# Kernel tuning notes

Hardware: AMD Instinct MI355X
Metric: run time of the kernel (lower is better)

Reference implementation:

```python
import jax, jax.numpy as jnp
import numpy as np

N, D, K = 32768, 256, 2048
BETA = 0.25  # init arg beta, in [0,1) branch of the loss


def setup_inputs() -> dict:
    key = jax.random.key(0)
    k1, k2 = jax.random.split(key)
    x = jax.random.normal(k1, (N, D), dtype=jnp.float32)
    # mimics nn.Embedding init: uniform(-1/K, 1/K) then mean-centered
    cb = jax.random.uniform(k2, (K, D), dtype=jnp.float32, minval=-1.0 / K, maxval=1.0 / K)
    codebook = cb - cb.mean(axis=0)
    return {"x": x, "codebook": codebook}


def reference(x, codebook):
    # pairwise squared L2 distances: [N, K]
    dist = (
        jnp.sum(x * x, axis=1, keepdims=True)
        + jnp.sum(codebook * codebook, axis=1)
        - 2.0 * jnp.matmul(x, codebook.T)
    )
    encoding_inds = jnp.argmin(dist, axis=1)  # [N]
    # one-hot @ codebook == gather of nearest code vectors
    x_codebook = jnp.take(codebook, encoding_inds, axis=0)  # [N, D]
    # straight-through quantization
    x_quantized = x + jax.lax.stop_gradient(x_codebook - x)
    # VQ loss, beta in [0, 1) branch
    commit = jnp.mean((x - jax.lax.stop_gradient(x_codebook)) ** 2)
    embed = jnp.mean((x_codebook - jax.lax.stop_gradient(x)) ** 2)
    loss = BETA * commit + embed
    return x_quantized, loss
```

## Files before the change

### kernel.cpp

```cpp
#include <hip/hip_runtime.h>

#define N_ROWS 32768
#define DIM    256
#define KCODES 2048
#define CSCALE 4096.0f

typedef __attribute__((ext_vector_type(16))) float f32x16;
typedef __attribute__((ext_vector_type(4)))  unsigned int u32x4;

union frag16 { u32x4 v; long l[2]; };

__device__ __forceinline__ void gl16(const void* g, void* l) {
    __builtin_amdgcn_global_load_lds(
        (const __attribute__((address_space(1))) unsigned int*)g,
        (__attribute__((address_space(3))) unsigned int*)l, 16, 0, 0);
}

__device__ __forceinline__ uint4 pack16(const float* s) {
    int a = __builtin_amdgcn_cvt_pk_fp8_f32(s[0],  s[1],  0, false);
    a     = __builtin_amdgcn_cvt_pk_fp8_f32(s[2],  s[3],  a, true);
    int b = __builtin_amdgcn_cvt_pk_fp8_f32(s[4],  s[5],  0, false);
    b     = __builtin_amdgcn_cvt_pk_fp8_f32(s[6],  s[7],  b, true);
    int c = __builtin_amdgcn_cvt_pk_fp8_f32(s[8],  s[9],  0, false);
    c     = __builtin_amdgcn_cvt_pk_fp8_f32(s[10], s[11], c, true);
    int d = __builtin_amdgcn_cvt_pk_fp8_f32(s[12], s[13], 0, false);
    d     = __builtin_amdgcn_cvt_pk_fp8_f32(s[14], s[15], d, true);
    uint4 o; o.x = a; o.y = b; o.z = c; o.w = d;
    return o;
}


__global__ void prep_cb(const float* __restrict__ cb, unsigned int* __restrict__ cbf8,
                        float* __restrict__ halfcn, float* __restrict__ loss) {
    const int t    = threadIdx.x;
    const int code = blockIdx.x * 4 + (t >> 6);
    const int s    = t & 63;
    if (blockIdx.x == 0 && t == 0) *loss = 0.0f;
    const int kc = s >> 4, d = (s >> 2) & 3, b4 = (s & 3) * 4;
    const int h = d >> 1, q = d & 1;
    const int k0 = kc * 64 + q * 32 + (b4 >> 3) * 16 + h * 8 + (b4 & 7);
    float4 v = *(const float4*)&cb[(size_t)code * DIM + k0];
    int pk = __builtin_amdgcn_cvt_pk_fp8_f32(v.x * CSCALE, v.y * CSCALE, 0, false);
    pk     = __builtin_amdgcn_cvt_pk_fp8_f32(v.z * CSCALE, v.w * CSCALE, pk, true);
    cbf8[(size_t)code * 64 + s] = (unsigned int)pk;
    float ssum = v.x * v.x + v.y * v.y + v.z * v.z + v.w * v.w;
    #pragma unroll
    for (int o = 32; o > 0; o >>= 1) ssum += __shfl_down(ssum, o, 64);
    if (s == 0) halfcn[code] = 0.5f * CSCALE * ssum;
}

__global__ __launch_bounds__(256, 3) void vq_fused(
        const float* __restrict__ x, const float* __restrict__ cb,
        const char* __restrict__ cbf8, const float* __restrict__ halfcn,
        float* __restrict__ out, float* __restrict__ loss) {
    __shared__ char As[4][4096];
    __shared__ char Bs[2][16384];
    __shared__ float red[64][4];
    __shared__ int  idxs[64];
    __shared__ float lred[4];

    const int t    = threadIdx.x;
    const int lane = t & 63;
    const int w    = t >> 6;
    const int l32  = lane & 31;
    const int h    = lane >> 5;
    const int row0 = blockIdx.x * 64;

    {
        const int r   = t >> 2;
        const int kc  = t & 3;
        const int key = (r >> 1) & 3;
        const float* src = x + (size_t)(row0 + r) * DIM + kc * 64;
        float buf[16];
        #pragma unroll
        for (int p = 0; p < 4; p++) {
            const int d = p ^ key, hh = d >> 1, qq = d & 1;
            #pragma unroll
            for (int j = 0; j < 4; j++) *(float4*)(buf + j * 4) =
                *(const float4*)(src + qq * 32 + (j >> 1) * 16 + hh * 8 + (j & 1) * 4);
            *(uint4*)(As[kc] + r * 64 + p * 16) = pack16(buf);
        }
    }

    auto stageB = [&](int pass, int kc, char* buf) {
        #pragma unroll
        for (int r_ = 0; r_ < 4; r_++) {
            const int lc = r_ * 64 + w * 16 + (lane >> 2);
            const int g  = (lane & 3) ^ ((lc >> 1) & 3);
            const char* src = cbf8 + (size_t)(pass * 256 + lc) * 256 + kc * 64 + g * 16;
            gl16(src, buf + (r_ * 64 + w * 16) * 64);
        }
    };

    float mp[2][16];
    #pragma unroll
    for (int rt = 0; rt < 2; rt++)
        #pragma unroll
        for (int r = 0; r < 16; r++) mp[rt][r] = -3.0e38f;

    const int key = (l32 >> 1) & 3;
    const int p0  = (h * 2 + 0) ^ key;
    const int p1  = (h * 2 + 1) ^ key;

    stageB(0, 0, Bs[0]);
    int cur = 0;
    for (int pass = 0; pass < 8; ++pass) {
        const float hc0 = halfcn[pass * 256 + w * 64 + l32];
        const float hc1 = halfcn[pass * 256 + w * 64 + 32 + l32];
        f32x16 acc[2][2];
        #pragma unroll
        for (int rt = 0; rt < 2; rt++)
            #pragma unroll
            for (int r = 0; r < 16; r++) { acc[rt][0][r] = -hc0; acc[rt][1][r] = -hc1; }

        #pragma unroll
        for (int kc = 0; kc < 4; ++kc) {
            __syncthreads();
            const int i = pass * 4 + kc;
            if (i < 31) stageB((i + 1) >> 2, (i + 1) & 3, Bs[cur ^ 1]);

            const char* ab = As[kc];
            const char* bb = Bs[cur];
            frag16 af[2][2], bf[2][2];
            #pragma unroll
            for (int rt = 0; rt < 2; rt++) {
                const int rbase = (rt * 32 + l32) * 64;
                af[rt][0].v = *(const u32x4*)(ab + rbase + p0 * 16);
                af[rt][1].v = *(const u32x4*)(ab + rbase + p1 * 16);
            }
            #pragma unroll
            for (int ct = 0; ct < 2; ct++) {
                const int cbase = (w * 64 + ct * 32 + l32) * 64;
                bf[ct][0].v = *(const u32x4*)(bb + cbase + p0 * 16);
                bf[ct][1].v = *(const u32x4*)(bb + cbase + p1 * 16);
            }
            #pragma unroll
            for (int q = 0; q < 2; q++)
                #pragma unroll
                for (int hf = 0; hf < 2; hf++)
                    #pragma unroll
                    for (int rt = 0; rt < 2; rt++)
                        #pragma unroll
                        for (int ct = 0; ct < 2; ct++)
                            acc[rt][ct] = __builtin_amdgcn_mfma_f32_32x32x16_fp8_fp8(
                                af[rt][q].l[hf], bf[ct][q].l[hf], acc[rt][ct], 0, 0, 0);
            cur ^= 1;
        }

        #pragma unroll
        for (int ct = 0; ct < 2; ct++) {
            const unsigned code = (unsigned)(pass * 256 + w * 64 + ct * 32 + l32);
            #pragma unroll
            for (int rt = 0; rt < 2; rt++)
                #pragma unroll
                for (int r = 0; r < 16; r++) {
                    unsigned u = (__float_as_uint(acc[rt][ct][r]) & 0xFFFFF800u) | code;
                    mp[rt][r] = fmaxf(mp[rt][r], __uint_as_float(u));
                }
        }
    }

    #pragma unroll
    for (int m = 1; m <= 16; m <<= 1)
        #pragma unroll
        for (int rt = 0; rt < 2; rt++)
            #pragma unroll
            for (int r = 0; r < 16; r++)
                mp[rt][r] = fmaxf(mp[rt][r], __shfl_xor(mp[rt][r], m, 64));

    if (l32 == 0) {
        #pragma unroll
        for (int rt = 0; rt < 2; rt++)
            #pragma unroll
            for (int r = 0; r < 16; r++) {
                const int row = rt * 32 + (r & 3) + 8 * (r >> 2) + 4 * h;
                red[row][w] = mp[rt][r];
            }
    }
    __syncthreads();
    if (t < 64) {
        float b0 = fmaxf(fmaxf(red[t][0], red[t][1]), fmaxf(red[t][2], red[t][3]));
        idxs[t] = (int)(__float_as_uint(b0) & 2047u);
    }
    __syncthreads();

    float lsum = 0.0f;
    #pragma unroll 4
    for (int r = 0; r < 64; r++) {
        const int code = idxs[r];
        const float c  = cb[(size_t)code * DIM + t];
        const float xv = x[(size_t)(row0 + r) * DIM + t];
        out[(size_t)(row0 + r) * DIM + t] = c;
        const float d = xv - c;
        lsum += d * d;
    }
    #pragma unroll
    for (int o = 32; o > 0; o >>= 1) lsum += __shfl_down(lsum, o, 64);
    if (lane == 0) lred[w] = lsum;
    __syncthreads();
    if (t == 0) {
        const float scale = 1.25f / (float)((size_t)N_ROWS * DIM);
        atomicAdd(loss, (lred[0] + lred[1] + lred[2] + lred[3]) * scale);
    }
}

extern "C" void kernel_launch(void* const* d_in, const int* in_sizes, int n_in,
                              void* d_out, int out_size, void* d_ws, size_t ws_size,
                              hipStream_t stream) {
    const float* x  = (const float*)d_in[0];
    const float* cb = (const float*)d_in[1];
    float* out  = (float*)d_out;
    float* loss = out + (size_t)N_ROWS * DIM;

    char* ws = (char*)d_ws;
    unsigned int* cbf8 = (unsigned int*)ws;
    float* halfcn = (float*)(ws + (size_t)KCODES * 256);

    prep_cb<<<KCODES / 4, 256, 0, stream>>>(cb, cbf8, halfcn, loss);
    vq_fused<<<N_ROWS / 64, 256, 0, stream>>>(x, cb, (const char*)cbf8, halfcn, out, loss);
}
```

Baseline: 126.0 us.

## Give each wave a private codebook slice and replace barriers with waitcnts

Each wave now stages only the 64 codebook rows it consumes into its own LDS region, so the per-k-chunk __syncthreads can be replaced by explicit s_waitcnt on vmcnt/lgkmcnt. The halfcn values for all passes are preloaded into registers up front, and launch bounds drop from 3 to 2 waves per SIMD to make room for the extra registers. The aim is to remove block-wide barrier stalls from the main MFMA loop. In exchange it lowers possible occupancy and depends on hand-encoded waitcnt constants being correct for the double buffer, with no barrier protecting against overwriting a buffer before the LDS reads are done.

```diff
diff --git a/kernel.cpp b/kernel.cpp
--- a/kernel.cpp
+++ b/kernel.cpp
@@ -9,6 +9,10 @@
 typedef __attribute__((ext_vector_type(4)))  unsigned int u32x4;
 
 union frag16 { u32x4 v; long l[2]; };
+
+#define WAIT_LGKM0 0xC07F
+#define WAIT_VM4   0x0F74
+#define WAIT_VM0   0x0F70
 
 __device__ __forceinline__ void gl16(const void* g, void* l) {
     __builtin_amdgcn_global_load_lds(
@@ -49,12 +53,12 @@
     if (s == 0) halfcn[code] = 0.5f * CSCALE * ssum;
 }
 
-__global__ __launch_bounds__(256, 3) void vq_fused(
+__global__ __launch_bounds__(256, 2) void vq_fused(
         const float* __restrict__ x, const float* __restrict__ cb,
         const char* __restrict__ cbf8, const float* __restrict__ halfcn,
         float* __restrict__ out, float* __restrict__ loss) {
     __shared__ char As[4][4096];
-    __shared__ char Bs[2][16384];
+    __shared__ char Bs[2][4][4096];
     __shared__ float red[64][4];
     __shared__ int  idxs[64];
     __shared__ float lred[4];
@@ -82,13 +86,25 @@
         }
     }
 
-    auto stageB = [&](int pass, int kc, char* buf) {
+    float hcv[8][2];
+    #pragma unroll
+    for (int p = 0; p < 8; p++) {
+        hcv[p][0] = halfcn[p * 256 + w * 64 + l32];
+        hcv[p][1] = halfcn[p * 256 + w * 64 + 32 + l32];
+    }
+
+    const int lsub = lane >> 2;
+    const int lpos = lane & 3;
+    auto stageB = [&](int i) {
+        const int pass = i >> 2, kc = i & 3;
+        char* dst = Bs[i & 1][w];
         #pragma unroll
         for (int r_ = 0; r_ < 4; r_++) {
-            const int lc = r_ * 64 + w * 16 + (lane >> 2);
-            const int g  = (lane & 3) ^ ((lc >> 1) & 3);
-            const char* src = cbf8 + (size_t)(pass * 256 + lc) * 256 + kc * 64 + g * 16;
-            gl16(src, buf + (r_ * 64 + w * 16) * 64);
+            const int lc = r_ * 16 + lsub;
+            const int g  = lpos ^ ((lc >> 1) & 3);
+            const char* src = cbf8 + (size_t)(pass * 256 + w * 64 + lc) * 256
+                              + kc * 64 + g * 16;
+            gl16(src, dst + r_ * 1024);
         }
     };
 
@@ -102,25 +118,32 @@
     const int p0  = (h * 2 + 0) ^ key;
     const int p1  = (h * 2 + 1) ^ key;
 
-    stageB(0, 0, Bs[0]);
-    int cur = 0;
+    __syncthreads();
+    stageB(0);
+
     for (int pass = 0; pass < 8; ++pass) {
-        const float hc0 = halfcn[pass * 256 + w * 64 + l32];
-        const float hc1 = halfcn[pass * 256 + w * 64 + 32 + l32];
         f32x16 acc[2][2];
         #pragma unroll
         for (int rt = 0; rt < 2; rt++)
             #pragma unroll
-            for (int r = 0; r < 16; r++) { acc[rt][0][r] = -hc0; acc[rt][1][r] = -hc1; }
+            for (int r = 0; r < 16; r++) {
+                acc[rt][0][r] = -hcv[pass][0];
+                acc[rt][1][r] = -hcv[pass][1];
+            }
 
         #pragma unroll
         for (int kc = 0; kc < 4; ++kc) {
-            __syncthreads();
             const int i = pass * 4 + kc;
-            if (i < 31) stageB((i + 1) >> 2, (i + 1) & 3, Bs[cur ^ 1]);
+            __builtin_amdgcn_s_waitcnt(WAIT_LGKM0);
+            if (i < 31) {
+                stageB(i + 1);
+                __builtin_amdgcn_s_waitcnt(WAIT_VM4);
+            } else {
+                __builtin_amdgcn_s_waitcnt(WAIT_VM0);
+            }
 
             const char* ab = As[kc];
-            const char* bb = Bs[cur];
+            const char* bb = Bs[i & 1][w];
             frag16 af[2][2], bf[2][2];
             #pragma unroll
             for (int rt = 0; rt < 2; rt++) {
@@ -130,7 +153,7 @@
             }
             #pragma unroll
             for (int ct = 0; ct < 2; ct++) {
-                const int cbase = (w * 64 + ct * 32 + l32) * 64;
+                const int cbase = (ct * 32 + l32) * 64;
                 bf[ct][0].v = *(const u32x4*)(bb + cbase + p0 * 16);
                 bf[ct][1].v = *(const u32x4*)(bb + cbase + p1 * 16);
             }
@@ -144,7 +167,6 @@
                         for (int ct = 0; ct < 2; ct++)
                             acc[rt][ct] = __builtin_amdgcn_mfma_f32_32x32x16_fp8_fp8(
                                 af[rt][q].l[hf], bf[ct][q].l[hf], acc[rt][ct], 0, 0, 0);
-            cur ^= 1;
         }
 
         #pragma unroll
```

Result: faster. 123.4 us (-2.0%).

## Split VQ into fp8 x prep, register-resident codebook argmin, and gather/loss kernels

Applied to the files above, without the earlier changes.

Replaces the single fused kernel with four. A separate kernel pre-converts x to fp8 in the output buffer. A codebook-stationary argmin kernel keeps 128 codes per block in registers and streams row tiles of x directly from global memory, with no LDS and no barriers, writing per-slot partial maxima. A finish kernel reduces the 64 partial slots per row, then does the gather, output write and loss. This removes LDS staging and sync overhead from the GEMM loop, but adds extra launches and global traffic for the fp8 copy of x and the partial buffer.

```diff
diff --git a/kernel.cpp b/kernel.cpp
--- a/kernel.cpp
+++ b/kernel.cpp
@@ -4,30 +4,13 @@
 #define DIM    256
 #define KCODES 2048
 #define CSCALE 4096.0f
+#define CG     16
+#define YS     48
+#define NSLOT  (CG * 4)
 
 typedef __attribute__((ext_vector_type(16))) float f32x16;
 typedef __attribute__((ext_vector_type(4)))  unsigned int u32x4;
-
 union frag16 { u32x4 v; long l[2]; };
-
-__device__ __forceinline__ void gl16(const void* g, void* l) {
-    __builtin_amdgcn_global_load_lds(
-        (const __attribute__((address_space(1))) unsigned int*)g,
-        (__attribute__((address_space(3))) unsigned int*)l, 16, 0, 0);
-}
-
-__device__ __forceinline__ uint4 pack16(const float* s) {
-    int a = __builtin_amdgcn_cvt_pk_fp8_f32(s[0],  s[1],  0, false);
-    a     = __builtin_amdgcn_cvt_pk_fp8_f32(s[2],  s[3],  a, true);
-    int b = __builtin_amdgcn_cvt_pk_fp8_f32(s[4],  s[5],  0, false);
-    b     = __builtin_amdgcn_cvt_pk_fp8_f32(s[6],  s[7],  b, true);
-    int c = __builtin_amdgcn_cvt_pk_fp8_f32(s[8],  s[9],  0, false);
-    c     = __builtin_amdgcn_cvt_pk_fp8_f32(s[10], s[11], c, true);
-    int d = __builtin_amdgcn_cvt_pk_fp8_f32(s[12], s[13], 0, false);
-    d     = __builtin_amdgcn_cvt_pk_fp8_f32(s[14], s[15], d, true);
-    uint4 o; o.x = a; o.y = b; o.z = c; o.w = d;
-    return o;
-}
 
 
 __global__ void prep_cb(const float* __restrict__ cb, unsigned int* __restrict__ cbf8,
@@ -49,144 +32,119 @@
     if (s == 0) halfcn[code] = 0.5f * CSCALE * ssum;
 }
 
-__global__ __launch_bounds__(256, 3) void vq_fused(
-        const float* __restrict__ x, const float* __restrict__ cb,
-        const char* __restrict__ cbf8, const float* __restrict__ halfcn,
-        float* __restrict__ out, float* __restrict__ loss) {
-    __shared__ char As[4][4096];
-    __shared__ char Bs[2][16384];
-    __shared__ float red[64][4];
-    __shared__ int  idxs[64];
-    __shared__ float lred[4];
+__global__ void prep_x(const float* __restrict__ x, unsigned int* __restrict__ x8) {
+    const int t   = threadIdx.x;
+    const int row = blockIdx.x * 4 + (t >> 6);
+    const int s   = t & 63;
+    const int kc = s >> 4, d = (s >> 2) & 3, b4 = (s & 3) * 4;
+    const int h = d >> 1, q = d & 1;
+    const int k0 = kc * 64 + q * 32 + (b4 >> 3) * 16 + h * 8 + (b4 & 7);
+    float4 v = *(const float4*)&x[(size_t)row * DIM + k0];
+    int pk = __builtin_amdgcn_cvt_pk_fp8_f32(v.x, v.y, 0, false);
+    pk     = __builtin_amdgcn_cvt_pk_fp8_f32(v.z, v.w, pk, true);
+    x8[(size_t)row * 64 + s] = (unsigned int)pk;
+}
 
+__global__ __launch_bounds__(256, 3) void vq_argmin(
+        const char* __restrict__ x8, const char* __restrict__ cbf8,
+        const float* __restrict__ halfcn, float* __restrict__ part) {
     const int t    = threadIdx.x;
     const int lane = t & 63;
     const int w    = t >> 6;
     const int l32  = lane & 31;
     const int h    = lane >> 5;
-    const int row0 = blockIdx.x * 64;
+    const int cg   = blockIdx.x;
+    const int by   = blockIdx.y;
+    const int code0 = cg * 128 + w * 32;
 
+    frag16 cf[4][2];
     {
-        const int r   = t >> 2;
-        const int kc  = t & 3;
-        const int key = (r >> 1) & 3;
-        const float* src = x + (size_t)(row0 + r) * DIM + kc * 64;
-        float buf[16];
+        const char* cbase = cbf8 + (size_t)(code0 + l32) * DIM;
         #pragma unroll
-        for (int p = 0; p < 4; p++) {
-            const int d = p ^ key, hh = d >> 1, qq = d & 1;
+        for (int kc = 0; kc < 4; kc++)
             #pragma unroll
-            for (int j = 0; j < 4; j++) *(float4*)(buf + j * 4) =
-                *(const float4*)(src + qq * 32 + (j >> 1) * 16 + hh * 8 + (j & 1) * 4);
-            *(uint4*)(As[kc] + r * 64 + p * 16) = pack16(buf);
-        }
+            for (int q = 0; q < 2; q++)
+                cf[kc][q].v = *(const u32x4*)(cbase + kc * 64 + (h * 2 + q) * 16);
     }
 
-    auto stageB = [&](int pass, int kc, char* buf) {
+    float bias[16];
+    #pragma unroll
+    for (int g = 0; g < 4; g++)
+        *(float4*)&bias[g * 4] = *(const float4*)&halfcn[code0 + g * 8 + 4 * h];
+
+    const unsigned codebase = (unsigned)(code0 + 4 * h);
+
+    const int s0 = (by * 512) / YS;
+    const int s1 = ((by + 1) * 512) / YS;
+
+    for (int s = s0; s < s1; ++s) {
+        const int r0 = s * 64;
+        frag16 xf[2][4][2];
+        const char* xb0 = x8 + (size_t)(r0 + l32) * DIM;
+        const char* xb1 = x8 + (size_t)(r0 + 32 + l32) * DIM;
         #pragma unroll
-        for (int r_ = 0; r_ < 4; r_++) {
-            const int lc = r_ * 64 + w * 16 + (lane >> 2);
-            const int g  = (lane & 3) ^ ((lc >> 1) & 3);
-            const char* src = cbf8 + (size_t)(pass * 256 + lc) * 256 + kc * 64 + g * 16;
-            gl16(src, buf + (r_ * 64 + w * 16) * 64);
+        for (int kc = 0; kc < 4; kc++)
+            #pragma unroll
+            for (int q = 0; q < 2; q++) {
+                xf[0][kc][q].v = *(const u32x4*)(xb0 + kc * 64 + (h * 2 + q) * 16);
+                xf[1][kc][q].v = *(const u32x4*)(xb1 + kc * 64 + (h * 2 + q) * 16);
+            }
+
+        f32x16 acc[2];
+        #pragma unroll
+        for (int r = 0; r < 16; r++) {
+            acc[0][r] = -bias[r];
+            acc[1][r] = -bias[r];
         }
-    };
-
-    float mp[2][16];
-    #pragma unroll
-    for (int rt = 0; rt < 2; rt++)
-        #pragma unroll
-        for (int r = 0; r < 16; r++) mp[rt][r] = -3.0e38f;
-
-    const int key = (l32 >> 1) & 3;
-    const int p0  = (h * 2 + 0) ^ key;
-    const int p1  = (h * 2 + 1) ^ key;
-
-    stageB(0, 0, Bs[0]);
-    int cur = 0;
-    for (int pass = 0; pass < 8; ++pass) {
-        const float hc0 = halfcn[pass * 256 + w * 64 + l32];
-        const float hc1 = halfcn[pass * 256 + w * 64 + 32 + l32];
-        f32x16 acc[2][2];
-        #pragma unroll
-        for (int rt = 0; rt < 2; rt++)
-            #pragma unroll
-            for (int r = 0; r < 16; r++) { acc[rt][0][r] = -hc0; acc[rt][1][r] = -hc1; }
 
         #pragma unroll
-        for (int kc = 0; kc < 4; ++kc) {
-            __syncthreads();
-            const int i = pass * 4 + kc;
-            if (i < 31) stageB((i + 1) >> 2, (i + 1) & 3, Bs[cur ^ 1]);
-
-            const char* ab = As[kc];
-            const char* bb = Bs[cur];
-            frag16 af[2][2], bf[2][2];
-            #pragma unroll
-            for (int rt = 0; rt < 2; rt++) {
-                const int rbase = (rt * 32 + l32) * 64;
-                af[rt][0].v = *(const u32x4*)(ab + rbase + p0 * 16);
-                af[rt][1].v = *(const u32x4*)(ab + rbase + p1 * 16);
-            }
-            #pragma unroll
-            for (int ct = 0; ct < 2; ct++) {
-                const int cbase = (w * 64 + ct * 32 + l32) * 64;
-                bf[ct][0].v = *(const u32x4*)(bb + cbase + p0 * 16);
-                bf[ct][1].v = *(const u32x4*)(bb + cbase + p1 * 16);
-            }
+        for (int kc = 0; kc < 4; kc++)
             #pragma unroll
             for (int q = 0; q < 2; q++)
                 #pragma unroll
-                for (int hf = 0; hf < 2; hf++)
+                for (int sl = 0; sl < 2; sl++)
                     #pragma unroll
                     for (int rt = 0; rt < 2; rt++)
-                        #pragma unroll
-                        for (int ct = 0; ct < 2; ct++)
-                            acc[rt][ct] = __builtin_amdgcn_mfma_f32_32x32x16_fp8_fp8(
-                                af[rt][q].l[hf], bf[ct][q].l[hf], acc[rt][ct], 0, 0, 0);
-            cur ^= 1;
-        }
+                        acc[rt] = __builtin_amdgcn_mfma_f32_32x32x16_fp8_fp8(
+                            cf[kc][q].l[sl], xf[rt][kc][q].l[sl], acc[rt], 0, 0, 0);
 
         #pragma unroll
-        for (int ct = 0; ct < 2; ct++) {
-            const unsigned code = (unsigned)(pass * 256 + w * 64 + ct * 32 + l32);
+        for (int rt = 0; rt < 2; rt++) {
+            float best = -3.0e38f;
             #pragma unroll
-            for (int rt = 0; rt < 2; rt++)
-                #pragma unroll
-                for (int r = 0; r < 16; r++) {
-                    unsigned u = (__float_as_uint(acc[rt][ct][r]) & 0xFFFFF800u) | code;
-                    mp[rt][r] = fmaxf(mp[rt][r], __uint_as_float(u));
-                }
+            for (int r = 0; r < 16; r++) {
+                const unsigned code = codebase + (unsigned)((r & 3) + 8 * (r >> 2));
+                const unsigned u = (__float_as_uint(acc[rt][r]) & 0xFFFFF800u) | code;
+                best = fmaxf(best, __uint_as_float(u));
+            }
+            best = fmaxf(best, __shfl_xor(best, 32, 64));
+            if (h == 0)
+                part[(size_t)(cg * 4 + w) * N_ROWS + r0 + rt * 32 + l32] = best;
         }
     }
+}
 
-    #pragma unroll
-    for (int m = 1; m <= 16; m <<= 1)
-        #pragma unroll
-        for (int rt = 0; rt < 2; rt++)
-            #pragma unroll
-            for (int r = 0; r < 16; r++)
-                mp[rt][r] = fmaxf(mp[rt][r], __shfl_xor(mp[rt][r], m, 64));
+__global__ void finish_kernel(const float* __restrict__ x, const float* __restrict__ cb,
+                              const float* __restrict__ part, float* __restrict__ out,
+                              float* __restrict__ loss) {
+    __shared__ int idxs[256];
+    __shared__ float lred[4];
+    const int t    = threadIdx.x;
+    const int row0 = blockIdx.x * 256;
 
-    if (l32 == 0) {
-        #pragma unroll
-        for (int rt = 0; rt < 2; rt++)
-            #pragma unroll
-            for (int r = 0; r < 16; r++) {
-                const int row = rt * 32 + (r & 3) + 8 * (r >> 2) + 4 * h;
-                red[row][w] = mp[rt][r];
-            }
-    }
-    __syncthreads();
-    if (t < 64) {
-        float b0 = fmaxf(fmaxf(red[t][0], red[t][1]), fmaxf(red[t][2], red[t][3]));
-        idxs[t] = (int)(__float_as_uint(b0) & 2047u);
+    {
+        const int row = row0 + t;
+        float best = part[row];
+        #pragma unroll 8
+        for (int sl = 1; sl < NSLOT; sl++)
+            best = fmaxf(best, part[(size_t)sl * N_ROWS + row]);
+        idxs[t] = (int)(__float_as_uint(best) & 2047u);
     }
     __syncthreads();
 
     float lsum = 0.0f;
     #pragma unroll 4
-    for (int r = 0; r < 64; r++) {
+    for (int r = 0; r < 256; r++) {
         const int code = idxs[r];
         const float c  = cb[(size_t)code * DIM + t];
         const float xv = x[(size_t)(row0 + r) * DIM + t];
@@ -196,7 +154,7 @@
     }
     #pragma unroll
     for (int o = 32; o > 0; o >>= 1) lsum += __shfl_down(lsum, o, 64);
-    if (lane == 0) lred[w] = lsum;
+    if ((t & 63) == 0) lred[t >> 6] = lsum;
     __syncthreads();
     if (t == 0) {
         const float scale = 1.25f / (float)((size_t)N_ROWS * DIM);
@@ -212,10 +170,16 @@
     float* out  = (float*)d_out;
     float* loss = out + (size_t)N_ROWS * DIM;
 
+    unsigned int* x8 = (unsigned int*)d_out;
+
     char* ws = (char*)d_ws;
     unsigned int* cbf8 = (unsigned int*)ws;
     float* halfcn = (float*)(ws + (size_t)KCODES * 256);
+    float* part   = (float*)(ws + (size_t)KCODES * 256 + 8192);
 
     prep_cb<<<KCODES / 4, 256, 0, stream>>>(cb, cbf8, halfcn, loss);
-    vq_fused<<<N_ROWS / 64, 256, 0, stream>>>(x, cb, (const char*)cbf8, halfcn, out, loss);
+    prep_x<<<N_ROWS / 4, 256, 0, stream>>>(x, x8);
+    vq_argmin<<<dim3(CG, YS), 256, 0, stream>>>((const char*)x8, (const char*)cbf8,
+                                                halfcn, part);
+    finish_kernel<<<N_ROWS / 256, 256, 0, stream>>>(x, cb, part, out, loss);
 }
```

New measurement: 184.8 us. 1.47x slower.

## Keep x fragments in registers and stream codebook directly into registers

Applied to the files above, without the earlier changes.

The fp8 x tile is loaded once from LDS into registers for the whole kernel, and codebook fragments are now read from global memory straight into double-buffered registers instead of being staged through LDS with syncthreads each chunk. The MFMA operands are swapped so codes lie along rows and x rows along columns. That lets each lane keep a single running max per row tile, which removes the 32-wide shuffle reduction. LDS use and barriers drop sharply, but occupancy is lowered to 2 waves per SIMD and each wave now issues uncoalesced-ish global loads without LDS sharing across waves.

```diff
diff --git a/kernel.cpp b/kernel.cpp
--- a/kernel.cpp
+++ b/kernel.cpp
@@ -7,14 +7,7 @@
 
 typedef __attribute__((ext_vector_type(16))) float f32x16;
 typedef __attribute__((ext_vector_type(4)))  unsigned int u32x4;
-
 union frag16 { u32x4 v; long l[2]; };
-
-__device__ __forceinline__ void gl16(const void* g, void* l) {
-    __builtin_amdgcn_global_load_lds(
-        (const __attribute__((address_space(1))) unsigned int*)g,
-        (__attribute__((address_space(3))) unsigned int*)l, 16, 0, 0);
-}
 
 __device__ __forceinline__ uint4 pack16(const float* s) {
     int a = __builtin_amdgcn_cvt_pk_fp8_f32(s[0],  s[1],  0, false);
@@ -49,15 +42,11 @@
     if (s == 0) halfcn[code] = 0.5f * CSCALE * ssum;
 }
 
-__global__ __launch_bounds__(256, 3) void vq_fused(
+__global__ __launch_bounds__(256, 2) void vq_fused(
         const float* __restrict__ x, const float* __restrict__ cb,
         const char* __restrict__ cbf8, const float* __restrict__ halfcn,
         float* __restrict__ out, float* __restrict__ loss) {
-    __shared__ char As[4][4096];
-    __shared__ char Bs[2][16384];
-    __shared__ float red[64][4];
-    __shared__ int  idxs[64];
-    __shared__ float lred[4];
+    __shared__ char mem[16384];
 
     const int t    = threadIdx.x;
     const int lane = t & 63;
@@ -78,108 +67,101 @@
             #pragma unroll
             for (int j = 0; j < 4; j++) *(float4*)(buf + j * 4) =
                 *(const float4*)(src + qq * 32 + (j >> 1) * 16 + hh * 8 + (j & 1) * 4);
-            *(uint4*)(As[kc] + r * 64 + p * 16) = pack16(buf);
+            *(uint4*)(mem + kc * 4096 + r * 64 + p * 16) = pack16(buf);
         }
     }
-
-    auto stageB = [&](int pass, int kc, char* buf) {
-        #pragma unroll
-        for (int r_ = 0; r_ < 4; r_++) {
-            const int lc = r_ * 64 + w * 16 + (lane >> 2);
-            const int g  = (lane & 3) ^ ((lc >> 1) & 3);
-            const char* src = cbf8 + (size_t)(pass * 256 + lc) * 256 + kc * 64 + g * 16;
-            gl16(src, buf + (r_ * 64 + w * 16) * 64);
+    __syncthreads();
+
+    const int key = (l32 >> 1) & 3;
+    frag16 xf[2][4][2];
+    #pragma unroll
+    for (int rt = 0; rt < 2; rt++)
+        #pragma unroll
+        for (int kc = 0; kc < 4; kc++)
+            #pragma unroll
+            for (int q = 0; q < 2; q++)
+                xf[rt][kc][q].v = *(const u32x4*)(mem + kc * 4096
+                    + (rt * 32 + l32) * 64 + (((h * 2 + q) ^ key)) * 16);
+    __syncthreads();
+
+    frag16 cf[2][4][2];
+    float  bias[2][16];
+    {
+        const char* cbase = cbf8 + (size_t)(w * 32 + l32) * DIM;
+        #pragma unroll
+        for (int kc = 0; kc < 4; kc++)
+            #pragma unroll
+            for (int q = 0; q < 2; q++)
+                cf[0][kc][q].v = *(const u32x4*)(cbase + kc * 64 + (h * 2 + q) * 16);
+        #pragma unroll
+        for (int g4 = 0; g4 < 4; g4++)
+            *(float4*)&bias[0][g4 * 4] = *(const float4*)&halfcn[w * 32 + g4 * 8 + 4 * h];
+    }
+
+    float mp[2] = {-3.0e38f, -3.0e38f};
+
+    #pragma unroll 2
+    for (int g = 0; g < 16; ++g) {
+        const int cur = g & 1, nxt = cur ^ 1;
+        if (g < 15) {
+            const char* cbase = cbf8 + (size_t)((g + 1) * 128 + w * 32 + l32) * DIM;
+            #pragma unroll
+            for (int kc = 0; kc < 4; kc++)
+                #pragma unroll
+                for (int q = 0; q < 2; q++)
+                    cf[nxt][kc][q].v = *(const u32x4*)(cbase + kc * 64 + (h * 2 + q) * 16);
+            #pragma unroll
+            for (int g4 = 0; g4 < 4; g4++)
+                *(float4*)&bias[nxt][g4 * 4] =
+                    *(const float4*)&halfcn[(g + 1) * 128 + w * 32 + g4 * 8 + 4 * h];
         }
-    };
-
-    float mp[2][16];
-    #pragma unroll
-    for (int rt = 0; rt < 2; rt++)
-        #pragma unroll
-        for (int r = 0; r < 16; r++) mp[rt][r] = -3.0e38f;
-
-    const int key = (l32 >> 1) & 3;
-    const int p0  = (h * 2 + 0) ^ key;
-    const int p1  = (h * 2 + 1) ^ key;
-
-    stageB(0, 0, Bs[0]);
-    int cur = 0;
-    for (int pass = 0; pass < 8; ++pass) {
-        const float hc0 = halfcn[pass * 256 + w * 64 + l32];
-        const float hc1 = halfcn[pass * 256 + w * 64 + 32 + l32];
-        f32x16 acc[2][2];
-        #pragma unroll
-        for (int rt = 0; rt < 2; rt++)
-            #pragma unroll
-            for (int r = 0; r < 16; r++) { acc[rt][0][r] = -hc0; acc[rt][1][r] = -hc1; }
-
-        #pragma unroll
-        for (int kc = 0; kc < 4; ++kc) {
-            __syncthreads();
-            const int i = pass * 4 + kc;
-            if (i < 31) stageB((i + 1) >> 2, (i + 1) & 3, Bs[cur ^ 1]);
-
-            const char* ab = As[kc];
-            const char* bb = Bs[cur];
-            frag16 af[2][2], bf[2][2];
-            #pragma unroll
-            for (int rt = 0; rt < 2; rt++) {
-                const int rbase = (rt * 32 + l32) * 64;
-                af[rt][0].v = *(const u32x4*)(ab + rbase + p0 * 16);
-                af[rt][1].v = *(const u32x4*)(ab + rbase + p1 * 16);
-            }
-            #pragma unroll
-            for (int ct = 0; ct < 2; ct++) {
-                const int cbase = (w * 64 + ct * 32 + l32) * 64;
-                bf[ct][0].v = *(const u32x4*)(bb + cbase + p0 * 16);
-                bf[ct][1].v = *(const u32x4*)(bb + cbase + p1 * 16);
-            }
+
+        f32x16 acc[2];
+        #pragma unroll
+        for (int r = 0; r < 16; r++) { acc[0][r] = -bias[cur][r]; acc[1][r] = -bias[cur][r]; }
+
+        #pragma unroll
+        for (int kc = 0; kc < 4; kc++)
             #pragma unroll
             for (int q = 0; q < 2; q++)
                 #pragma unroll
-                for (int hf = 0; hf < 2; hf++)
+                for (int sl = 0; sl < 2; sl++)
                     #pragma unroll
                     for (int rt = 0; rt < 2; rt++)
-                        #pragma unroll
-                        for (int ct = 0; ct < 2; ct++)
-                            acc[rt][ct] = __builtin_amdgcn_mfma_f32_32x32x16_fp8_fp8(
-                                af[rt][q].l[hf], bf[ct][q].l[hf], acc[rt][ct], 0, 0, 0);
-            cur ^= 1;
+                        acc[rt] = __builtin_amdgcn_mfma_f32_32x32x16_fp8_fp8(
+                            cf[cur][kc][q].l[sl], xf[rt][kc][q].l[sl], acc[rt], 0, 0, 0);
+
+        const unsigned codebase = (unsigned)(g * 128 + w * 32 + 4 * h);
+        #pragma unroll
+        for (int rt = 0; rt < 2; rt++) {
+            float best = mp[rt];
+            #pragma unroll
+            for (int r = 0; r < 16; r++) {
+                const unsigned code = codebase + (unsigned)((r & 3) + 8 * (r >> 2));
+                const unsigned u = (__float_as_uint(acc[rt][r]) & 0xFFFFF800u) | code;
+                best = fmaxf(best, __uint_as_float(u));
+            }
+            mp[rt] = best;
         }
-
-        #pragma unroll
-        for (int ct = 0; ct < 2; ct++) {
-            const unsigned code = (unsigned)(pass * 256 + w * 64 + ct * 32 + l32);
-            #pragma unroll
-            for (int rt = 0; rt < 2; rt++)
-                #pragma unroll
-                for (int r = 0; r < 16; r++) {
-                    unsigned u = (__float_as_uint(acc[rt][ct][r]) & 0xFFFFF800u) | code;
-                    mp[rt][r] = fmaxf(mp[rt][r], __uint_as_float(u));
-                }
-        }
-    }
-
-    #pragma unroll
-    for (int m = 1; m <= 16; m <<= 1)
-        #pragma unroll
-        for (int rt = 0; rt < 2; rt++)
-            #pragma unroll
-            for (int r = 0; r < 16; r++)
-                mp[rt][r] = fmaxf(mp[rt][r], __shfl_xor(mp[rt][r], m, 64));
-
-    if (l32 == 0) {
-        #pragma unroll
-        for (int rt = 0; rt < 2; rt++)
-            #pragma unroll
-            for (int r = 0; r < 16; r++) {
-                const int row = rt * 32 + (r & 3) + 8 * (r >> 2) + 4 * h;
-                red[row][w] = mp[rt][r];
-            }
+    }
+
+    #pragma unroll
+    for (int rt = 0; rt < 2; rt++)
+        mp[rt] = fmaxf(mp[rt], __shfl_xor(mp[rt], 32, 64));
+
+    __syncthreads();
+    float* red  = (float*)mem;
+    int*   idxs = (int*)(mem + 1024);
+    float* lred = (float*)(mem + 1280);
+
+    if (h == 0) {
+        red[(l32)      * 4 + w] = mp[0];
+        red[(32 + l32) * 4 + w] = mp[1];
     }
     __syncthreads();
     if (t < 64) {
-        float b0 = fmaxf(fmaxf(red[t][0], red[t][1]), fmaxf(red[t][2], red[t][3]));
+        float b0 = fmaxf(fmaxf(red[t * 4 + 0], red[t * 4 + 1]),
+                         fmaxf(red[t * 4 + 2], red[t * 4 + 3]));
         idxs[t] = (int)(__float_as_uint(b0) & 2047u);
     }
     __syncthreads();
```

New measurement: 131.0 us. 1.04x slower.
